# Performance work log

Hardware: AMD Instinct MI355X
Metric: run time of the kernel (lower is better)

The kernel has to match this reference:

```python
import jax, jax.numpy as jnp
import numpy as np


def conv2d(x, w, b, pad):
    y = jax.lax.conv_general_dilated(x, w, (1, 1), [(pad, pad), (pad, pad)],
                                     dimension_numbers=('NCHW', 'OIHW', 'NCHW'))
    return y + b[None, :, None, None]


def setup_inputs() -> dict:
    key = jax.random.key(0)
    ks = jax.random.split(key, 24)
    bs, C, OC, K = 2, 64, 3, 3
    hi = wi = 96
    ho = wo = 192

    def _w(k, o, i, kh, kw):
        return jax.random.normal(k, (o, i, kh, kw), jnp.float32) / np.float32(np.sqrt(i * kh * kw))

    inp = {
        'x': jax.random.normal(ks[0], (bs, C, hi, wi), jnp.float32),
        'poseMap': jax.random.normal(ks[1], (1, 3, ho, wo), jnp.float32),
        'interMapY': jax.random.randint(ks[2], (ho, wo), 0, hi, jnp.int32),
        'interMapX': jax.random.randint(ks[3], (ho, wo), 0, wi, jnp.int32),
        # sigmaconv: 3x3 convs 64->64->64->2
        'sig_w1': _w(ks[4], 64, 64, 3, 3), 'sig_b1': jnp.zeros((64,), jnp.float32),
        'sig_w2': _w(ks[5], 64, 64, 3, 3), 'sig_b2': jnp.zeros((64,), jnp.float32),
        'sig_w3': _w(ks[6], 2, 64, 3, 3), 'sig_b3': jnp.zeros((2,), jnp.float32),
        # dwconv: 1x1 convs 3->64->256->C*K*K
        'dw_w1': _w(ks[7], 64, 3, 1, 1), 'dw_b1': jnp.zeros((64,), jnp.float32),
        'dw_w2': _w(ks[8], 256, 64, 1, 1), 'dw_b2': jnp.zeros((256,), jnp.float32),
        'dw_w3': _w(ks[9], C * K * K, 256, 1, 1), 'dw_b3': jnp.zeros((C * K * K,), jnp.float32),
        # pwconv: 1x1 convs 3->64->256->C*OC
        'pw_w1': _w(ks[10], 64, 3, 1, 1), 'pw_b1': jnp.zeros((64,), jnp.float32),
        'pw_w2': _w(ks[11], 256, 64, 1, 1), 'pw_b2': jnp.zeros((256,), jnp.float32),
        'pw_w3': _w(ks[12], C * OC, 256, 1, 1), 'pw_b3': jnp.zeros((C * OC,), jnp.float32),
    }
    return inp


def reference(x, poseMap, interMapY, interMapX,
              sig_w1, sig_b1, sig_w2, sig_b2, sig_w3, sig_b3,
              dw_w1, dw_b1, dw_w2, dw_b2, dw_w3, dw_b3,
              pw_w1, pw_b1, pw_w2, pw_b2, pw_w3, pw_b3):
    C, K, OC = 64, 3, 3
    bs, _, hi, wi = x.shape
    ho, wo = poseMap.shape[2], poseMap.shape[3]
    pad = K // 2

    p = jax.lax.stop_gradient(poseMap)  # original detaches poseMap
    # kernel-predict branches (1x1 conv MLPs over position map)
    dw = conv2d(jax.nn.relu(conv2d(jax.nn.relu(conv2d(p, dw_w1, dw_b1, 0)), dw_w2, dw_b2, 0)), dw_w3, dw_b3, 0)
    dw = dw.reshape(1, C, K * K, ho, wo)
    pw = conv2d(jax.nn.relu(conv2d(jax.nn.relu(conv2d(p, pw_w1, pw_b1, 0)), pw_w2, pw_b2, 0)), pw_w3, pw_b3, 0)
    pw = pw.reshape(C, OC, ho, wo)

    # unfold(x, K, padding=K//2): [bs, C, K*K, hi, wi], kernel taps row-major
    xp = jnp.pad(x, ((0, 0), (0, 0), (pad, pad), (pad, pad)))
    h = jnp.stack([xp[:, :, dy:dy + hi, dx:dx + wi]
                   for dy in range(K) for dx in range(K)], axis=2)
    # irregular spatial gather to HR grid: [bs, C, K*K, ho, wo]
    h = h[:, :, :, interMapY, interMapX]

    mean = jnp.sum(h * jax.nn.softmax(dw, axis=2), axis=2)  # [bs, C, ho, wo]
    sigma = conv2d(jax.nn.relu(conv2d(jax.nn.relu(conv2d(mean, sig_w1, sig_b1, 1)), sig_w2, sig_b2, 1)), sig_w3, sig_b3, 1)
    sigmad = sigma[:, 0:1, None, :, :]
    sigmar = sigma[:, 1:2, None, :, :]
    bw = sigmad * dw + sigmar * jnp.abs(h - mean[:, :, None, :, :])
    xa = jnp.sum(h * jax.nn.softmax(bw, axis=2), axis=2)  # [bs, C, ho, wo]
    out = jnp.einsum('bchw,cohw->bohw', xa, pw)  # [bs, OC, ho, wo]
    return out
```

## Files before the change

### kernel.cpp

```cpp
#include <hip/hip_runtime.h>

#define NPIX 36864

typedef __attribute__((ext_vector_type(8))) short short8;
typedef __attribute__((ext_vector_type(4))) short short4v;
typedef __attribute__((ext_vector_type(4))) float float4v;

__device__ inline unsigned short f2b(float x) {
    unsigned int u = __float_as_uint(x);
    unsigned int r = (u + 0x7FFFu + ((u >> 16) & 1u)) >> 16;
    return (unsigned short)r;
}
__device__ inline float b2f(unsigned short h) {
    return __uint_as_float(((unsigned int)h) << 16);
}

#define WB_TOTAL 312320
#define XCAST_N  1179648
__global__ __launch_bounds__(256) void prep_all(
    const float* __restrict__ dw2, const float* __restrict__ dw3,
    const float* __restrict__ pw2, const float* __restrict__ pw3,
    const float* __restrict__ sw1, const float* __restrict__ sw2,
    const float* __restrict__ sw3, unsigned short* __restrict__ wb,
    const float* __restrict__ x, unsigned short* __restrict__ xb)
{
    int i = blockIdx.x * 256 + threadIdx.x;
    if (i >= WB_TOTAL) {
        int j = i - WB_TOTAL;
        if (j < XCAST_N) xb[j] = f2b(x[j]);
        return;
    }
    unsigned short v;
    if (i < 16384)        v = f2b(dw2[i]);
    else if (i < 32768)   v = f2b(pw2[i - 16384]);
    else if (i < 180224)  v = f2b(dw3[i - 32768]);
    else if (i < 229376)  v = f2b(pw3[i - 180224]);
    else if (i < 266240) { int j = i - 229376; int t = j / 4096, r = j % 4096, oc = r / 64, ic = r % 64;
                           v = f2b(sw1[(oc * 64 + ic) * 9 + t]); }
    else if (i < 303104) { int j = i - 266240; int t = j / 4096, r = j % 4096, oc = r / 64, ic = r % 64;
                           v = f2b(sw2[(oc * 64 + ic) * 9 + t]); }
    else                 { int j = i - 303104; int t = j / 1024, r = j % 1024, oc = r / 64, ic = r % 64;
                           v = (oc < 2) ? f2b(sw3[(oc * 64 + ic) * 9 + t]) : (unsigned short)0; }
    wb[i] = v;
}

__global__ __launch_bounds__(256) void l1_k(
    const float* __restrict__ pose,
    const float* __restrict__ wA, const float* __restrict__ bA,
    const float* __restrict__ wB, const float* __restrict__ bB,
    unsigned short* __restrict__ out)
{
    int px = blockIdx.x * 256 + threadIdx.x;
    int chain = blockIdx.y;
    int cg = blockIdx.z * 16;
    const float* w = chain ? wB : wA;
    const float* bi = chain ? bB : bA;
    float p0 = pose[px], p1 = pose[NPIX + px], p2 = pose[2 * NPIX + px];
    unsigned int pk[8];
    #pragma unroll
    for (int c = 0; c < 16; ++c) {
        int cc = cg + c;
        float v = bi[cc] + w[cc * 3] * p0 + w[cc * 3 + 1] * p1 + w[cc * 3 + 2] * p2;
        v = fmaxf(v, 0.f);
        unsigned short u = f2b(v);
        if (c & 1) pk[c >> 1] |= ((unsigned int)u) << 16; else pk[c >> 1] = u;
    }
    uint4* o = (uint4*)&out[((size_t)chain * NPIX + px) * 64 + cg];
    o[0] = ((uint4*)pk)[0];
    o[1] = ((uint4*)pk)[1];
}

template<int K>
__global__ __launch_bounds__(256) void gemm_dual(
    const unsigned short* __restrict__ actA, const unsigned short* __restrict__ actB,
    const unsigned short* __restrict__ wgtA, const unsigned short* __restrict__ wgtB,
    const float* __restrict__ biasA, const float* __restrict__ biasB,
    unsigned short* __restrict__ outA, unsigned short* __restrict__ outB,
    int tilesA, int octotA, int octotB, int relu)
{
    constexpr int KP = K + 8;
    constexpr int NK = K / 32;
    __shared__ unsigned short Bs[64 * KP];
    const int tid = threadIdx.x;
    const int px0 = blockIdx.x * 64;
    const bool second = (int)blockIdx.y >= tilesA;
    const int oc0 = (second ? blockIdx.y - tilesA : blockIdx.y) * 64;
    const unsigned short* act = second ? actB : actA;
    const unsigned short* wgt = second ? wgtB : wgtA;
    const float* bias = second ? biasB : biasA;
    unsigned short* outp = second ? outB : outA;
    const int octot = second ? octotB : octotA;
    const int w = tid >> 6, l = tid & 63;
    const int ln = l & 15, lkg = l >> 4, lk = lkg * 8;
    const int ocA = oc0 + w * 16 + ln;
    short8 Ar[NK];
    #pragma unroll
    for (int kc = 0; kc < NK; ++kc)
        Ar[kc] = *(const short8*)&wgt[(size_t)ocA * K + kc * 32 + lk];
    for (int idx = tid; idx < 64 * (K / 8); idx += 256) {
        int p = idx / (K / 8), ko = (idx % (K / 8)) * 8;
        *(short8*)&Bs[p * KP + ko] = *(const short8*)&act[(size_t)(px0 + p) * K + ko];
    }
    __syncthreads();
    float4v acc[4] = {{0,0,0,0},{0,0,0,0},{0,0,0,0},{0,0,0,0}};
    #pragma unroll
    for (int kc = 0; kc < NK; ++kc) {
        #pragma unroll
        for (int nt = 0; nt < 4; ++nt) {
            short8 b = *(const short8*)&Bs[(nt * 16 + ln) * KP + kc * 32 + lk];
            acc[nt] = __builtin_amdgcn_mfma_f32_16x16x32_bf16(Ar[kc], b, acc[nt], 0, 0, 0);
        }
    }
    #pragma unroll
    for (int nt = 0; nt < 4; ++nt) {
        int px = px0 + nt * 16 + ln;
        int oc = oc0 + w * 16 + lkg * 4;
        float v[4];
        #pragma unroll
        for (int r = 0; r < 4; ++r) {
            v[r] = acc[nt][r] + bias[oc + r];
            if (relu) v[r] = fmaxf(v[r], 0.f);
        }
        uint2 pk;
        pk.x = (unsigned int)f2b(v[0]) | (((unsigned int)f2b(v[1])) << 16);
        pk.y = (unsigned int)f2b(v[2]) | (((unsigned int)f2b(v[3])) << 16);
        *(uint2*)&outp[(size_t)px * octot + oc] = pk;
    }
}

__global__ __launch_bounds__(256) void gemm_l3(
    const unsigned short* __restrict__ actA, const unsigned short* __restrict__ actB,
    const unsigned short* __restrict__ wgt,
    const float* __restrict__ biasA, const float* __restrict__ biasB,
    unsigned short* __restrict__ outA, unsigned short* __restrict__ outB)
{
    __shared__ unsigned short Bs[64 * 264];
    unsigned short* Ts = Bs;
    const int tid = threadIdx.x;
    const int px0 = blockIdx.x * 64;
    const int mb  = blockIdx.y;
    const unsigned short* act = (mb < 3) ? actA : actB;
    const int w = tid >> 6, l = tid & 63;
    const int ln = l & 15, lkg = l >> 4, lk = lkg * 8;
    const int row0 = mb * 192 + w * 48 + ln;
    short8 Ar[3][8];
    #pragma unroll
    for (int mt = 0; mt < 3; ++mt)
        #pragma unroll
        for (int kc = 0; kc < 8; ++kc)
            Ar[mt][kc] = *(const short8*)&wgt[(size_t)(row0 + mt * 16) * 256 + kc * 32 + lk];
    for (int idx = tid; idx < 64 * 32; idx += 256) {
        int p = idx >> 5, ko = (idx & 31) * 8;
        *(short8*)&Bs[p * 264 + ko] = *(const short8*)&act[(size_t)(px0 + p) * 256 + ko];
    }
    __syncthreads();
    float4v acc[3][4] = {};
    #pragma unroll
    for (int kc = 0; kc < 8; ++kc) {
        #pragma unroll
        for (int nt = 0; nt < 4; ++nt) {
            short8 b = *(const short8*)&Bs[(nt * 16 + ln) * 264 + kc * 32 + lk];
            acc[0][nt] = __builtin_amdgcn_mfma_f32_16x16x32_bf16(Ar[0][kc], b, acc[0][nt], 0, 0, 0);
            acc[1][nt] = __builtin_amdgcn_mfma_f32_16x16x32_bf16(Ar[1][kc], b, acc[1][nt], 0, 0, 0);
            acc[2][nt] = __builtin_amdgcn_mfma_f32_16x16x32_bf16(Ar[2][kc], b, acc[2][nt], 0, 0, 0);
        }
    }
    __syncthreads();
    #pragma unroll
    for (int mt = 0; mt < 3; ++mt) {
        #pragma unroll
        for (int nt = 0; nt < 4; ++nt) {
            int col = nt * 16 + ln;
            #pragma unroll
            for (int r = 0; r < 4; ++r) {
                int row = w * 48 + mt * 16 + lkg * 4 + r;
                int goc = mb * 192 + row;
                float bv = (goc < 576) ? biasA[goc] : biasB[goc - 576];
                Ts[row * 72 + col] = f2b(acc[mt][nt][r] + bv);
            }
        }
    }
    __syncthreads();
    for (int i = tid; i < 1536; i += 256) {
        int row = i >> 3, ch = (i & 7) * 8;
        int goc = mb * 192 + row;
        unsigned short* dst = (goc < 576) ? (outA + (size_t)goc * NPIX)
                                          : (outB + (size_t)(goc - 576) * NPIX);
        *(short8*)&dst[px0 + ch] = *(const short8*)&Ts[row * 72 + ch];
    }
}

template<int MT>
__global__ __launch_bounds__(256) void conv3x3_mfma(
    const unsigned short* __restrict__ act, const unsigned short* __restrict__ wgt,
    const float* __restrict__ bias, unsigned short* __restrict__ out,
    int relu)
{
    constexpr int SP = 72;
    constexpr int OCP = MT * 16;
    __shared__ unsigned short Bs[3 * 66 * SP];
    const int tid = threadIdx.x;
    int bx = blockIdx.x;
    const int xt = bx % 3; bx /= 3;
    const int y = bx % 192; const int b = bx / 192;
    const int x0 = xt * 64;
    const size_t actb = (size_t)b * NPIX * 64;
    const int w = tid >> 6, l = tid & 63;
    const int ln = l & 15, lkg = l >> 4, lk = lkg * 8;
    const int mt = (MT == 4) ? w : 0;
    short8 Wr[9][2];
    #pragma unroll
    for (int t = 0; t < 9; ++t)
        #pragma unroll
        for (int hh = 0; hh < 2; ++hh)
            Wr[t][hh] = *(const short8*)&wgt[((size_t)t * OCP + mt * 16 + ln) * 64 + hh * 32 + lk];
    for (int s = tid; s < 198; s += 256) {
        int r = s / 66, i = s % 66;
        int yy = y + r - 1, xx = x0 + i - 1;
        unsigned short* dst = &Bs[(r * 66 + i) * SP];
        if (yy >= 0 && yy < 192 && xx >= 0 && xx < 192) {
            const unsigned short* src = &act[actb + (size_t)(yy * 192 + xx) * 64];
            #pragma unroll
            for (int j = 0; j < 8; ++j) *(short8*)(dst + j * 8) = *(const short8*)(src + j * 8);
        } else {
            short8 z = {};
            #pragma unroll
            for (int j = 0; j < 8; ++j) *(short8*)(dst + j * 8) = z;
        }
    }
    __syncthreads();
    const int NT = (MT == 4) ? 4 : 1;
    const int ntb = (MT == 4) ? 0 : w;
    float4v acc[4] = {{0,0,0,0},{0,0,0,0},{0,0,0,0},{0,0,0,0}};
    #pragma unroll
    for (int t = 0; t < 9; ++t) {
        const int r = t / 3, dx = t % 3;
        #pragma unroll
        for (int hh = 0; hh < 2; ++hh) {
            #pragma unroll
            for (int n = 0; n < 4; ++n) {
                if (n >= NT) break;
                int slot = r * 66 + (ntb + n) * 16 + ln + dx;
                short8 bf = *(const short8*)&Bs[slot * SP + hh * 32 + lk];
                acc[n] = __builtin_amdgcn_mfma_f32_16x16x32_bf16(Wr[t][hh], bf, acc[n], 0, 0, 0);
            }
        }
    }
    #pragma unroll
    for (int n = 0; n < 4; ++n) {
        if (n >= NT) break;
        int px = y * 192 + x0 + (ntb + n) * 16 + ln;
        if (MT == 4) {
            int oc = mt * 16 + lkg * 4;
            float v0 = acc[n][0] + bias[oc + 0];
            float v1 = acc[n][1] + bias[oc + 1];
            float v2 = acc[n][2] + bias[oc + 2];
            float v3 = acc[n][3] + bias[oc + 3];
            if (relu) { v0 = fmaxf(v0, 0.f); v1 = fmaxf(v1, 0.f); v2 = fmaxf(v2, 0.f); v3 = fmaxf(v3, 0.f); }
            uint2 pk;
            pk.x = (unsigned int)f2b(v0) | (((unsigned int)f2b(v1)) << 16);
            pk.y = (unsigned int)f2b(v2) | (((unsigned int)f2b(v3)) << 16);
            *(uint2*)&out[((size_t)b * NPIX + px) * 64 + oc] = pk;
        } else if (lkg == 0) {
            float v0 = acc[n][0] + bias[0];
            float v1 = acc[n][1] + bias[1];
            out[((size_t)b * 2 + 0) * NPIX + px] = f2b(v0);
            out[((size_t)b * 2 + 1) * NPIX + px] = f2b(v1);
        }
    }
}

#define PLSZ 10192
__device__ inline void stage_planes(const unsigned short* __restrict__ xb, int c,
                                    unsigned short* __restrict__ pl, int tid)
{
    short8 z = {};
    short8* pf = (short8*)pl;
    for (int i = tid; i < (2 * PLSZ) / 8; i += 256) pf[i] = z;
    __syncthreads();
    #pragma unroll
    for (int b = 0; b < 2; ++b) {
        const unsigned short* xp = xb + (size_t)(b * 64 + c) * 9216;
        unsigned short* pb = pl + b * PLSZ;
        for (int i = tid; i < 96 * 12; i += 256) {
            int row = i / 12, ch = i % 12;
            const short4v* src = (const short4v*)&xp[row * 96 + ch * 8];
            unsigned short* d = &pb[(row + 1) * 104 + 4 + ch * 8];
            *(short4v*)d = src[0];
            *(short4v*)(d + 4) = src[1];
        }
    }
    __syncthreads();
}

__global__ __launch_bounds__(256) void mean_k(
    const unsigned short* __restrict__ xb, const int* __restrict__ imy, const int* __restrict__ imx,
    const unsigned short* __restrict__ dw, unsigned short* __restrict__ mean_cm)
{
    __shared__ unsigned short pl[2 * PLSZ];
    const int c = blockIdx.y;
    const int px0 = blockIdx.x * 1024;
    const int tid = threadIdx.x;
    stage_planes(xb, c, pl, tid);
    #pragma unroll
    for (int q = 0; q < 4; ++q) {
        int px = px0 + q * 256 + tid;
        int base = imy[px] * 104 + imx[px] + 3;
        float wk[9];
        {
            float d[9];
            #pragma unroll
            for (int k = 0; k < 9; ++k) d[k] = b2f(dw[(size_t)(c * 9 + k) * NPIX + px]);
            float m = d[0];
            #pragma unroll
            for (int k = 1; k < 9; ++k) m = fmaxf(m, d[k]);
            float s = 0.f;
            #pragma unroll
            for (int k = 0; k < 9; ++k) { wk[k] = __expf(d[k] - m); s += wk[k]; }
            float inv = 1.f / s;
            #pragma unroll
            for (int k = 0; k < 9; ++k) wk[k] *= inv;
        }
        #pragma unroll
        for (int b = 0; b < 2; ++b) {
            const unsigned short* pb = pl + b * PLSZ;
            float a = 0.f;
            #pragma unroll
            for (int k = 0; k < 9; ++k)
                a += wk[k] * b2f(pb[base + (k / 3) * 104 + (k % 3)]);
            mean_cm[(size_t)(b * 64 + c) * NPIX + px] = f2b(a);
        }
    }
}

__global__ __launch_bounds__(256) void tr_k(
    const unsigned short* __restrict__ in, unsigned short* __restrict__ out)
{
    __shared__ unsigned short T[64 * 68];
    int px0 = blockIdx.x * 64;
    int b = blockIdx.y;
    int tid = threadIdx.x;
    for (int i = tid; i < 4096; i += 256) {
        int c = i >> 6, p = i & 63;
        T[p * 68 + c] = in[(size_t)(b * 64 + c) * NPIX + px0 + p];
    }
    __syncthreads();
    for (int i = tid; i < 4096; i += 256) {
        int p = i >> 6, c = i & 63;
        out[((size_t)b * NPIX + px0 + p) * 64 + c] = T[p * 68 + c];
    }
}

__global__ __launch_bounds__(256) void xa_k(
    const unsigned short* __restrict__ xb, const int* __restrict__ imy, const int* __restrict__ imx,
    const unsigned short* __restrict__ dw, const unsigned short* __restrict__ mean_cm,
    const unsigned short* __restrict__ sigma, unsigned short* __restrict__ xab)
{
    __shared__ unsigned short pl[2 * PLSZ];
    const int c = blockIdx.y;
    const int px0 = blockIdx.x * 1024;
    const int tid = threadIdx.x;
    stage_planes(xb, c, pl, tid);
    #pragma unroll
    for (int q = 0; q < 4; ++q) {
        int px = px0 + q * 256 + tid;
        int base = imy[px] * 104 + imx[px] + 3;
        float d[9];
        #pragma unroll
        for (int k = 0; k < 9; ++k) d[k] = b2f(dw[(size_t)(c * 9 + k) * NPIX + px]);
        #pragma unroll
        for (int b = 0; b < 2; ++b) {
            const unsigned short* pb = pl + b * PLSZ;
            float mn = b2f(mean_cm[(size_t)(b * 64 + c) * NPIX + px]);
            float sd = b2f(sigma[((size_t)b * 2 + 0) * NPIX + px]);
            float sr = b2f(sigma[((size_t)b * 2 + 1) * NPIX + px]);
            float h[9], bw[9];
            #pragma unroll
            for (int k = 0; k < 9; ++k) {
                h[k] = b2f(pb[base + (k / 3) * 104 + (k % 3)]);
                bw[k] = sd * d[k] + sr * fabsf(h[k] - mn);
            }
            float m = bw[0];
            #pragma unroll
            for (int k = 1; k < 9; ++k) m = fmaxf(m, bw[k]);
            float s = 0.f, a = 0.f;
            #pragma unroll
            for (int k = 0; k < 9; ++k) { float e = __expf(bw[k] - m); s += e; a += e * h[k]; }
            xab[(size_t)(b * 64 + c) * NPIX + px] = f2b(a / s);
        }
    }
}

__global__ __launch_bounds__(256) void einsum_part(
    const unsigned short* __restrict__ xab, const unsigned short* __restrict__ pw,
    float* __restrict__ part)
{
    int px = blockIdx.x * 256 + threadIdx.x;
    int b = blockIdx.y;
    int c0 = blockIdx.z * 16;
    float a0 = 0.f, a1 = 0.f, a2 = 0.f;
    #pragma unroll
    for (int c = 0; c < 16; ++c) {
        float v = b2f(xab[(size_t)(b * 64 + c0 + c) * NPIX + px]);
        a0 += v * b2f(pw[(size_t)((c0 + c) * 3 + 0) * NPIX + px]);
        a1 += v * b2f(pw[(size_t)((c0 + c) * 3 + 1) * NPIX + px]);
        a2 += v * b2f(pw[(size_t)((c0 + c) * 3 + 2) * NPIX + px]);
    }
    size_t base = ((size_t)blockIdx.z * 6 + b * 3) * NPIX + px;
    part[base + 0 * NPIX] = a0;
    part[base + 1 * NPIX] = a1;
    part[base + 2 * NPIX] = a2;
}

__global__ __launch_bounds__(256) void einsum_red(
    const float* __restrict__ part, float* __restrict__ out)
{
    int i = blockIdx.x * 256 + threadIdx.x;
    float s = part[i] + part[(size_t)6 * NPIX + i] + part[(size_t)12 * NPIX + i] + part[(size_t)18 * NPIX + i];
    out[i] = s;
}

extern "C" void kernel_launch(void* const* d_in, const int* in_sizes, int n_in,
                              void* d_out, int out_size, void* d_ws, size_t ws_size,
                              hipStream_t stream)
{
    (void)in_sizes; (void)n_in; (void)out_size; (void)ws_size;
    const float* x      = (const float*)d_in[0];
    const float* pose   = (const float*)d_in[1];
    const int*   imy    = (const int*)d_in[2];
    const int*   imx    = (const int*)d_in[3];
    const float* sig_w1 = (const float*)d_in[4];
    const float* sig_b1 = (const float*)d_in[5];
    const float* sig_w2 = (const float*)d_in[6];
    const float* sig_b2 = (const float*)d_in[7];
    const float* sig_w3 = (const float*)d_in[8];
    const float* sig_b3 = (const float*)d_in[9];
    const float* dw_w1  = (const float*)d_in[10];
    const float* dw_b1  = (const float*)d_in[11];
    const float* dw_w2  = (const float*)d_in[12];
    const float* dw_b2  = (const float*)d_in[13];
    const float* dw_w3  = (const float*)d_in[14];
    const float* dw_b3  = (const float*)d_in[15];
    const float* pw_w1  = (const float*)d_in[16];
    const float* pw_b1  = (const float*)d_in[17];
    const float* pw_w2  = (const float*)d_in[18];
    const float* pw_b2  = (const float*)d_in[19];
    const float* pw_w3  = (const float*)d_in[20];
    const float* pw_b3  = (const float*)d_in[21];
    float* out = (float*)d_out;

    unsigned short* ws = (unsigned short*)d_ws;
    size_t off = 0;
    unsigned short* wb      = ws + off; off += WB_TOTAL;
    unsigned short* xb16    = ws + off; off += (size_t)XCAST_N;
    unsigned short* h1      = ws + off; off += (size_t)2 * NPIX * 64;
    unsigned short* h2      = ws + off; off += (size_t)2 * NPIX * 256;
    unsigned short* dwbuf   = ws + off; off += (size_t)576 * NPIX;
    unsigned short* pwbuf   = ws + off; off += (size_t)192 * NPIX;
    unsigned short* mean_cm = ws + off; off += (size_t)2 * 64 * NPIX;
    unsigned short* mean_pm = ws + off; off += (size_t)2 * NPIX * 64;
    unsigned short* s1      = ws + off; off += (size_t)2 * NPIX * 64;
    unsigned short* s2      = ws + off; off += (size_t)2 * NPIX * 64;
    unsigned short* sigma   = ws + off; off += (size_t)2 * 2 * NPIX;
    unsigned short* xab     = ws + off; off += (size_t)2 * 64 * NPIX;
    off = (off + 1) & ~(size_t)1;
    float* part = (float*)(ws + off);

    unsigned short* w_dw2 = wb + 0;
    unsigned short* w_pw2 = wb + 16384;
    unsigned short* w_33  = wb + 32768;
    unsigned short* w_s1t = wb + 229376;
    unsigned short* w_s2t = wb + 266240;
    unsigned short* w_s3t = wb + 303104;

    unsigned short* h1dw = h1;
    unsigned short* h1pw = h1 + (size_t)NPIX * 64;
    unsigned short* h2dw = h2;
    unsigned short* h2pw = h2 + (size_t)NPIX * 256;

    dim3 blk(256);
    prep_all<<<dim3((WB_TOTAL + XCAST_N + 255) / 256), blk, 0, stream>>>(
        dw_w2, dw_w3, pw_w2, pw_w3, sig_w1, sig_w2, sig_w3, wb, x, xb16);
    l1_k<<<dim3(144, 2, 4), blk, 0, stream>>>(pose, dw_w1, dw_b1, pw_w1, pw_b1, h1);
    gemm_dual<64><<<dim3(576, 8), blk, 0, stream>>>(
        h1dw, h1pw, w_dw2, w_pw2, dw_b2, pw_b2, h2dw, h2pw, 4, 256, 256, 1);
    gemm_l3<<<dim3(576, 4), blk, 0, stream>>>(
        h2dw, h2pw, w_33, dw_b3, pw_b3, dwbuf, pwbuf);
    mean_k<<<dim3(36, 64), blk, 0, stream>>>(xb16, imy, imx, dwbuf, mean_cm);
    tr_k<<<dim3(576, 2), blk, 0, stream>>>(mean_cm, mean_pm);
    conv3x3_mfma<4><<<dim3(1152), blk, 0, stream>>>(mean_pm, w_s1t, sig_b1, s1, 1);
    conv3x3_mfma<4><<<dim3(1152), blk, 0, stream>>>(s1,      w_s2t, sig_b2, s2, 1);
    conv3x3_mfma<1><<<dim3(1152), blk, 0, stream>>>(s2,      w_s3t, sig_b3, sigma, 0);
    xa_k<<<dim3(36, 64), blk, 0, stream>>>(xb16, imy, imx, dwbuf, mean_cm, sigma, xab);
    einsum_part<<<dim3(144, 2, 4), blk, 0, stream>>>(xab, pwbuf, part);
    einsum_red<<<dim3(864), blk, 0, stream>>>(part, out);
}
```

Measured before the change: 283.9 us.

## Enlarge pixel tiles in kernel-predict MLP GEMMs and stage outputs via LDS

The first layer now computes all 64 channels per thread instead of splitting channels over a grid dimension, so fewer blocks each reread the pose values. The 64->256 GEMM now handles 256 pixels per block and stages its output through shared memory for coalesced 16-byte stores. The 256->576 GEMM handles 128 pixels per block and loads weight fragments per k-chunk instead of preloading them all into registers. The aim is more weight reuse per block, fewer blocks, and better-coalesced stores, at the cost of more registers and shared memory per block, which may lower occupancy.

```diff
diff --git a/kernel.cpp b/kernel.cpp
--- a/kernel.cpp
+++ b/kernel.cpp
@@ -52,22 +52,20 @@
 {
     int px = blockIdx.x * 256 + threadIdx.x;
     int chain = blockIdx.y;
-    int cg = blockIdx.z * 16;
     const float* w = chain ? wB : wA;
     const float* bi = chain ? bB : bA;
     float p0 = pose[px], p1 = pose[NPIX + px], p2 = pose[2 * NPIX + px];
-    unsigned int pk[8];
-    #pragma unroll
-    for (int c = 0; c < 16; ++c) {
-        int cc = cg + c;
-        float v = bi[cc] + w[cc * 3] * p0 + w[cc * 3 + 1] * p1 + w[cc * 3 + 2] * p2;
+    unsigned int pk[32];
+    #pragma unroll
+    for (int c = 0; c < 64; ++c) {
+        float v = bi[c] + w[c * 3] * p0 + w[c * 3 + 1] * p1 + w[c * 3 + 2] * p2;
         v = fmaxf(v, 0.f);
         unsigned short u = f2b(v);
         if (c & 1) pk[c >> 1] |= ((unsigned int)u) << 16; else pk[c >> 1] = u;
     }
-    uint4* o = (uint4*)&out[((size_t)chain * NPIX + px) * 64 + cg];
-    o[0] = ((uint4*)pk)[0];
-    o[1] = ((uint4*)pk)[1];
+    uint4* o = (uint4*)&out[((size_t)chain * NPIX + px) * 64];
+    #pragma unroll
+    for (int q = 0; q < 8; ++q) o[q] = ((uint4*)pk)[q];
 }
 
 template<int K>
@@ -79,10 +77,10 @@
     int tilesA, int octotA, int octotB, int relu)
 {
     constexpr int KP = K + 8;
-    constexpr int NK = K / 32;
-    __shared__ unsigned short Bs[64 * KP];
+    __shared__ unsigned short Bs[256 * KP];
+    unsigned short* Ts = Bs;
     const int tid = threadIdx.x;
-    const int px0 = blockIdx.x * 64;
+    const int px0 = blockIdx.x * 256;
     const bool second = (int)blockIdx.y >= tilesA;
     const int oc0 = (second ? blockIdx.y - tilesA : blockIdx.y) * 64;
     const unsigned short* act = second ? actB : actA;
@@ -93,38 +91,41 @@
     const int w = tid >> 6, l = tid & 63;
     const int ln = l & 15, lkg = l >> 4, lk = lkg * 8;
     const int ocA = oc0 + w * 16 + ln;
-    short8 Ar[NK];
-    #pragma unroll
-    for (int kc = 0; kc < NK; ++kc)
-        Ar[kc] = *(const short8*)&wgt[(size_t)ocA * K + kc * 32 + lk];
-    for (int idx = tid; idx < 64 * (K / 8); idx += 256) {
-        int p = idx / (K / 8), ko = (idx % (K / 8)) * 8;
+    short8 Ar[2];
+    Ar[0] = *(const short8*)&wgt[(size_t)ocA * K + lk];
+    Ar[1] = *(const short8*)&wgt[(size_t)ocA * K + 32 + lk];
+    for (int idx = tid; idx < 256 * (K / 8); idx += 256) {
+        int p = idx >> 3, ko = (idx & 7) * 8;
         *(short8*)&Bs[p * KP + ko] = *(const short8*)&act[(size_t)(px0 + p) * K + ko];
     }
     __syncthreads();
-    float4v acc[4] = {{0,0,0,0},{0,0,0,0},{0,0,0,0},{0,0,0,0}};
-    #pragma unroll
-    for (int kc = 0; kc < NK; ++kc) {
-        #pragma unroll
-        for (int nt = 0; nt < 4; ++nt) {
+    float4v acc[16] = {};
+    #pragma unroll
+    for (int kc = 0; kc < 2; ++kc) {
+        #pragma unroll
+        for (int nt = 0; nt < 16; ++nt) {
             short8 b = *(const short8*)&Bs[(nt * 16 + ln) * KP + kc * 32 + lk];
             acc[nt] = __builtin_amdgcn_mfma_f32_16x16x32_bf16(Ar[kc], b, acc[nt], 0, 0, 0);
         }
     }
-    #pragma unroll
-    for (int nt = 0; nt < 4; ++nt) {
-        int px = px0 + nt * 16 + ln;
-        int oc = oc0 + w * 16 + lkg * 4;
-        float v[4];
+    __syncthreads();
+    float bv[4];
+    #pragma unroll
+    for (int r = 0; r < 4; ++r) bv[r] = bias[oc0 + w * 16 + lkg * 4 + r];
+    #pragma unroll
+    for (int nt = 0; nt < 16; ++nt) {
+        int pxl = nt * 16 + ln;
         #pragma unroll
         for (int r = 0; r < 4; ++r) {
-            v[r] = acc[nt][r] + bias[oc + r];
-            if (relu) v[r] = fmaxf(v[r], 0.f);
-        }
-        uint2 pk;
-        pk.x = (unsigned int)f2b(v[0]) | (((unsigned int)f2b(v[1])) << 16);
-        pk.y = (unsigned int)f2b(v[2]) | (((unsigned int)f2b(v[3])) << 16);
-        *(uint2*)&outp[(size_t)px * octot + oc] = pk;
+            float v = acc[nt][r] + bv[r];
+            if (relu) v = fmaxf(v, 0.f);
+            Ts[pxl * KP + w * 16 + lkg * 4 + r] = f2b(v);
+        }
+    }
+    __syncthreads();
+    for (int c = tid; c < 2048; c += 256) {
+        int pxl = c >> 3, ch = (c & 7) * 8;
+        *(short8*)&outp[(size_t)(px0 + pxl) * octot + oc0 + ch] = *(const short8*)&Ts[pxl * KP + ch];
     }
 }
 
@@ -134,59 +135,54 @@
     const float* __restrict__ biasA, const float* __restrict__ biasB,
     unsigned short* __restrict__ outA, unsigned short* __restrict__ outB)
 {
-    __shared__ unsigned short Bs[64 * 264];
+    __shared__ unsigned short Bs[128 * 264];
     unsigned short* Ts = Bs;
     const int tid = threadIdx.x;
-    const int px0 = blockIdx.x * 64;
+    const int px0 = blockIdx.x * 128;
     const int mb  = blockIdx.y;
     const unsigned short* act = (mb < 3) ? actA : actB;
     const int w = tid >> 6, l = tid & 63;
     const int ln = l & 15, lkg = l >> 4, lk = lkg * 8;
     const int row0 = mb * 192 + w * 48 + ln;
-    short8 Ar[3][8];
-    #pragma unroll
-    for (int mt = 0; mt < 3; ++mt)
-        #pragma unroll
-        for (int kc = 0; kc < 8; ++kc)
-            Ar[mt][kc] = *(const short8*)&wgt[(size_t)(row0 + mt * 16) * 256 + kc * 32 + lk];
-    for (int idx = tid; idx < 64 * 32; idx += 256) {
+    for (int idx = tid; idx < 128 * 32; idx += 256) {
         int p = idx >> 5, ko = (idx & 31) * 8;
         *(short8*)&Bs[p * 264 + ko] = *(const short8*)&act[(size_t)(px0 + p) * 256 + ko];
     }
     __syncthreads();
-    float4v acc[3][4] = {};
+    float4v acc[3][8] = {};
     #pragma unroll
     for (int kc = 0; kc < 8; ++kc) {
-        #pragma unroll
-        for (int nt = 0; nt < 4; ++nt) {
+        short8 a0 = *(const short8*)&wgt[(size_t)(row0 +  0) * 256 + kc * 32 + lk];
+        short8 a1 = *(const short8*)&wgt[(size_t)(row0 + 16) * 256 + kc * 32 + lk];
+        short8 a2 = *(const short8*)&wgt[(size_t)(row0 + 32) * 256 + kc * 32 + lk];
+        #pragma unroll
+        for (int nt = 0; nt < 8; ++nt) {
             short8 b = *(const short8*)&Bs[(nt * 16 + ln) * 264 + kc * 32 + lk];
-            acc[0][nt] = __builtin_amdgcn_mfma_f32_16x16x32_bf16(Ar[0][kc], b, acc[0][nt], 0, 0, 0);
-            acc[1][nt] = __builtin_amdgcn_mfma_f32_16x16x32_bf16(Ar[1][kc], b, acc[1][nt], 0, 0, 0);
-            acc[2][nt] = __builtin_amdgcn_mfma_f32_16x16x32_bf16(Ar[2][kc], b, acc[2][nt], 0, 0, 0);
+            acc[0][nt] = __builtin_amdgcn_mfma_f32_16x16x32_bf16(a0, b, acc[0][nt], 0, 0, 0);
+            acc[1][nt] = __builtin_amdgcn_mfma_f32_16x16x32_bf16(a1, b, acc[1][nt], 0, 0, 0);
+            acc[2][nt] = __builtin_amdgcn_mfma_f32_16x16x32_bf16(a2, b, acc[2][nt], 0, 0, 0);
         }
     }
     __syncthreads();
     #pragma unroll
     for (int mt = 0; mt < 3; ++mt) {
-        #pragma unroll
-        for (int nt = 0; nt < 4; ++nt) {
-            int col = nt * 16 + ln;
-            #pragma unroll
-            for (int r = 0; r < 4; ++r) {
-                int row = w * 48 + mt * 16 + lkg * 4 + r;
-                int goc = mb * 192 + row;
-                float bv = (goc < 576) ? biasA[goc] : biasB[goc - 576];
-                Ts[row * 72 + col] = f2b(acc[mt][nt][r] + bv);
-            }
-        }
-    }
-    __syncthreads();
-    for (int i = tid; i < 1536; i += 256) {
-        int row = i >> 3, ch = (i & 7) * 8;
+        int rowb = w * 48 + mt * 16 + lkg * 4;
+        #pragma unroll
+        for (int r = 0; r < 4; ++r) {
+            int goc = mb * 192 + rowb + r;
+            float bv = (goc < 576) ? biasA[goc] : biasB[goc - 576];
+            #pragma unroll
+            for (int nt = 0; nt < 8; ++nt)
+                Ts[(rowb + r) * 136 + nt * 16 + ln] = f2b(acc[mt][nt][r] + bv);
+        }
+    }
+    __syncthreads();
+    for (int c = tid; c < 3072; c += 256) {
+        int row = c >> 4, ch = (c & 15) * 8;
         int goc = mb * 192 + row;
         unsigned short* dst = (goc < 576) ? (outA + (size_t)goc * NPIX)
                                           : (outB + (size_t)(goc - 576) * NPIX);
-        *(short8*)&dst[px0 + ch] = *(const short8*)&Ts[row * 72 + ch];
+        *(short8*)&dst[px0 + ch] = *(const short8*)&Ts[row * 136 + ch];
     }
 }
 
@@ -481,10 +477,10 @@
     dim3 blk(256);
     prep_all<<<dim3((WB_TOTAL + XCAST_N + 255) / 256), blk, 0, stream>>>(
         dw_w2, dw_w3, pw_w2, pw_w3, sig_w1, sig_w2, sig_w3, wb, x, xb16);
-    l1_k<<<dim3(144, 2, 4), blk, 0, stream>>>(pose, dw_w1, dw_b1, pw_w1, pw_b1, h1);
-    gemm_dual<64><<<dim3(576, 8), blk, 0, stream>>>(
+    l1_k<<<dim3(144, 2), blk, 0, stream>>>(pose, dw_w1, dw_b1, pw_w1, pw_b1, h1);
+    gemm_dual<64><<<dim3(144, 8), blk, 0, stream>>>(
         h1dw, h1pw, w_dw2, w_pw2, dw_b2, pw_b2, h2dw, h2pw, 4, 256, 256, 1);
-    gemm_l3<<<dim3(576, 4), blk, 0, stream>>>(
+    gemm_l3<<<dim3(288, 4), blk, 0, stream>>>(
         h2dw, h2pw, w_33, dw_b3, pw_b3, dwbuf, pwbuf);
     mean_k<<<dim3(36, 64), blk, 0, stream>>>(xb16, imy, imx, dwbuf, mean_cm);
     tr_k<<<dim3(576, 2), blk, 0, stream>>>(mean_cm, mean_pm);
```

Result: faster. 277.2 us (-2.4%).
